# Kernel optimization log

Hardware: AMD Instinct MI355X
Metric: run time of the kernel (lower is better)

The kernel has to match this reference:

```python
import jax, jax.numpy as jnp
import numpy as np

STRIDE = 2

def setup_inputs() -> dict:
    key = jax.random.key(0)
    k1, k2 = jax.random.split(key)
    x = jax.random.normal(k1, (4, 64, 16, 16, 16), dtype=jnp.float32)
    weight = jax.random.normal(k2, (32, 64, 3, 3, 3), dtype=jnp.float32)
    return {"x": x, "weight": weight}


def reference(x, weight):
    # Faithful to ConvTranspose3dMPS.forward:
    # 1) nearest-neighbor upsample by `stride` via repeat
    # 2) per (out,in) channel pair: circular conv via FFT, summed over in
    B, C, D, H, W = x.shape
    s = STRIDE
    Co, Ci, k, _, _ = weight.shape
    Du, Hu, Wu = D * s, H * s, W * s

    # view->repeat->view == repeat each voxel s times along each spatial axis
    xu = jnp.repeat(jnp.repeat(jnp.repeat(x, s, axis=2), s, axis=3), s, axis=4)

    # FFT of upsampled input (computed once, not per channel pair)
    fx = jnp.fft.fftn(xu, axes=(2, 3, 4))  # [B, Ci, Du, Hu, Wu] complex

    # torch.fft.fftn(weight[i,j], s=x.shape[-3:]) zero-pads kernel at the end
    wpad = jnp.zeros((Co, Ci, Du, Hu, Wu), dtype=weight.dtype)
    wpad = wpad.at[:, :, :k, :k, :k].set(weight)
    fw = jnp.fft.fftn(wpad, axes=(2, 3, 4))  # [Co, Ci, Du, Hu, Wu] complex

    # sum over input channels in frequency domain, take real part of ifft
    fo = jnp.einsum('bjdhw,ijdhw->bidhw', fx, fw)
    out = jnp.fft.ifftn(fo, axes=(2, 3, 4)).real.astype(x.dtype)
    return out
```

## Files before the change

### kernel.cpp

```cpp
#include <hip/hip_runtime.h>


typedef float f32x16 __attribute__((ext_vector_type(16)));
typedef short s16x8 __attribute__((ext_vector_type(8)));

#define CI  64
#define CO  32
#define QV  4096
#define XT_ELEMS (4 * QV * CI)
#define WE_PP    (16 * 8 * 32 * 8)
#define WE_BYTES 65536
#define X_BYTES  81920
#define LDS_BYTES (WE_BYTES + X_BYTES)

__device__ __forceinline__ unsigned short f32_to_bf16_rne(float f) {
    union { float f; unsigned u; } v; v.f = f;
    unsigned u = v.u;
    unsigned r = u + 0x7FFFu + ((u >> 16) & 1u);
    return (unsigned short)(r >> 16);
}

__device__ __forceinline__ void gload_lds16(const void* g, void* l) {
    __builtin_amdgcn_global_load_lds(
        (__attribute__((address_space(1))) unsigned int*)g,
        (__attribute__((address_space(3))) unsigned int*)l, 16, 0, 0);
}

__global__ __launch_bounds__(256)
void prep_kernel(const float* __restrict__ x, const float* __restrict__ weight,
                 unsigned short* __restrict__ xT, unsigned short* __restrict__ WeG) {
    const int blk = blockIdx.x;
    {
        const int tid = blk * 256 + threadIdx.x;
        const int b  = tid >> 15;
        const int rem = tid & 32767;
        const int c  = rem >> 12;
        const int q  = rem & 4095;
        const float* xb = x + b * (CI * QV) + q;
        s16x8 pk;
        #pragma unroll
        for (int e = 0; e < 8; ++e)
            pk[e] = (short)f32_to_bf16_rne(xb[(c * 8 + e) * QV]);
        *reinterpret_cast<s16x8*>(xT + (((size_t)(b * 8 + c)) * QV + q) * 8) = pk;
    }
    if (threadIdx.x < 32) {
        const int tid = blk * 32 + threadIdx.x;
        const int p = tid >> 11, i = (tid >> 6) & 31, j = tid & 63;
        const int pd = p >> 2, ph = (p >> 1) & 1, pw = p & 1;
        const int pp = pd * 2 + ph;

        const float* wp = weight + (i * CI + j) * 27;
        float wv[27];
        #pragma unroll
        for (int k = 0; k < 27; ++k) wv[k] = wp[k];

        float t1[2][9];
        #pragma unroll
        for (int m = 0; m < 9; ++m) {
            t1[0][m] = pd ? (wv[m] + wv[9 + m]) : wv[m];
            t1[1][m] = pd ? wv[18 + m] : (wv[9 + m] + wv[18 + m]);
        }
        float t2[2][2][3];
        #pragma unroll
        for (int td = 0; td < 2; ++td)
            #pragma unroll
            for (int m = 0; m < 3; ++m) {
                t2[td][0][m] = ph ? (t1[td][m] + t1[td][3 + m]) : t1[td][m];
                t2[td][1][m] = ph ? (t1[td][6 + m]) : (t1[td][3 + m] + t1[td][6 + m]);
            }

        const int c = j >> 3, e = j & 7;
        #pragma unroll
        for (int td = 0; td < 2; ++td)
            #pragma unroll
            for (int th = 0; th < 2; ++th) {
                float a0 = pw ? (t2[td][th][0] + t2[td][th][1]) : t2[td][th][0];
                float a1 = pw ? t2[td][th][2] : (t2[td][th][1] + t2[td][th][2]);
                const int tA = td * 4 + th * 2;
                const int plane0 = pw * 8 + tA;
                WeG[(((pp * 16 + plane0) * 8 + c) * 32 + i) * 8 + e]     = f32_to_bf16_rne(a0);
                WeG[(((pp * 16 + plane0 + 1) * 8 + c) * 32 + i) * 8 + e] = f32_to_bf16_rne(a1);
            }
    }
}

__global__ __launch_bounds__(256)
void convt3d_mfma_kernel(const unsigned short* __restrict__ xT,
                         const unsigned short* __restrict__ WeG,
                         float* __restrict__ out) {
    __shared__ __align__(16) char smem[LDS_BYTES];
    unsigned short* we_lds = (unsigned short*)smem;
    char* x_lds = smem + WE_BYTES;

    const int blk = blockIdx.x;
    const int pp  = blk >> 6;
    const int T2  = blk & 63;
    const int pd = pp >> 1, ph = pp & 1;
    const int qd = T2 >> 2, qhq = T2 & 3;

    const int w    = threadIdx.x >> 6;
    const int lane = threadIdx.x & 63;

    {
        const char* src = (const char*)(WeG + pp * WE_PP);
        #pragma unroll
        for (int k = 0; k < 16; ++k) {
            const int off = (w * 16 + k) * 1024 + lane * 16;
            gload_lds16(src + off, smem + off);
        }
    }
    {
        const char* srcb = (const char*)xT;
        #pragma unroll
        for (int k = 0; k < 20; ++k) {
            const int chunk = w * 20 + k;
            const int seg   = chunk * 4 + (lane >> 4);
            const int bc    = seg / 10;
            const int dhh   = seg - bc * 10;
            const int dd_i  = (dhh >= 5) ? 1 : 0;
            const int hh_i  = dhh - dd_i * 5;
            const int dd = (qd - 1 + dd_i) & 15;
            const int hh = (qhq * 4 - 1 + hh_i) & 15;
            const long srcoff = ((long)bc * QV + (dd * 16 + hh) * 16 + (lane & 15)) * 16;
            gload_lds16(srcb + srcoff, x_lds + chunk * 1024 + lane * 16);
        }
    }
    asm volatile("s_waitcnt vmcnt(0)" ::: "memory");
    __syncthreads();

    const int b    = w;
    const int n    = lane & 31;
    const int half = lane >> 5;
    const int qw   = n & 15;
    const int hsel = n >> 4;

    f32x16 acc00 = {}, acc01 = {};
    f32x16 acc10 = {}, acc11 = {};

    #pragma unroll
    for (int t = 0; t < 8; ++t) {
        const int td = t >> 2, th = (t >> 1) & 1, tw = t & 1;
        const int dd_i = 1 - td;
        const int ww = (qw - tw) & 15;
        const int hbase = dd_i * 5 + hsel + 1 - th;
        #pragma unroll
        for (int ks = 0; ks < 4; ++ks) {
            const int c  = 2 * ks + half;
            const int bc = b * 8 + c;
            const s16x8 b0 = *reinterpret_cast<const s16x8*>(
                x_lds + (bc * 10 + hbase) * 256 + ww * 16);
            const s16x8 b1 = *reinterpret_cast<const s16x8*>(
                x_lds + (bc * 10 + hbase + 2) * 256 + ww * 16);
            const s16x8 a0 = *reinterpret_cast<const s16x8*>(
                we_lds + ((t * 8 + c) * 32 + n) * 8);
            const s16x8 a1 = *reinterpret_cast<const s16x8*>(
                we_lds + (((8 + t) * 8 + c) * 32 + n) * 8);
            acc00 = __builtin_amdgcn_mfma_f32_32x32x16_bf16(a0, b0, acc00, 0, 0, 0);
            acc01 = __builtin_amdgcn_mfma_f32_32x32x16_bf16(a1, b0, acc01, 0, 0, 0);
            acc10 = __builtin_amdgcn_mfma_f32_32x32x16_bf16(a0, b1, acc10, 0, 0, 0);
            acc11 = __builtin_amdgcn_mfma_f32_32x32x16_bf16(a1, b1, acc11, 0, 0, 0);
        }
    }

    const int d = 2 * qd + pd;
    #pragma unroll
    for (int tau = 0; tau < 2; ++tau) {
        const int h = 2 * (4 * qhq + 2 * tau + hsel) + ph;
        float* ob = out + ((size_t)b * CO) * 32768 + d * 1024 + h * 32 + 2 * qw;
        #pragma unroll
        for (int r = 0; r < 16; ++r) {
            const int m = (r & 3) + 8 * (r >> 2) + 4 * half;
            float2 v;
            if (tau == 0) { v.x = acc00[r]; v.y = acc01[r]; }
            else          { v.x = acc10[r]; v.y = acc11[r]; }
            *reinterpret_cast<float2*>(ob + (size_t)m * 32768) = v;
        }
    }
}

extern "C" void kernel_launch(void* const* d_in, const int* in_sizes, int n_in,
                              void* d_out, int out_size, void* d_ws, size_t ws_size,
                              hipStream_t stream) {
    const float* x      = (const float*)d_in[0];
    const float* weight = (const float*)d_in[1];
    float* out          = (float*)d_out;

    unsigned short* xT = (unsigned short*)d_ws;
    unsigned short* We = xT + XT_ELEMS;

    prep_kernel<<<512, 256, 0, stream>>>(x, weight, xT, We);
    convt3d_mfma_kernel<<<256, 256, 0, stream>>>(xT, We, out);
}
```

Before: 18.54 us.

## Fuse input/weight bf16 prep into the MFMA conv kernel, drop prep launch

Removes the separate prep kernel and the workspace round trip. Each block now reads fp32 weights and input directly, folds the weights into parity-phase form, converts to bf16 and writes both into LDS itself. This saves a kernel launch and the global write and read of the intermediate buffers. In exchange, each of the 256 blocks recomputes its weight fold (64 x 32 x 27 floats read per block) and does strided fp32 loads of x, which duplicates work and adds latency before the MFMA loop.

```diff
diff --git a/kernel.cpp b/kernel.cpp
--- a/kernel.cpp
+++ b/kernel.cpp
@@ -7,8 +7,6 @@
 #define CI  64
 #define CO  32
 #define QV  4096
-#define XT_ELEMS (4 * QV * CI)
-#define WE_PP    (16 * 8 * 32 * 8)
 #define WE_BYTES 65536
 #define X_BYTES  81920
 #define LDS_BYTES (WE_BYTES + X_BYTES)
@@ -20,74 +18,10 @@
     return (unsigned short)(r >> 16);
 }
 
-__device__ __forceinline__ void gload_lds16(const void* g, void* l) {
-    __builtin_amdgcn_global_load_lds(
-        (__attribute__((address_space(1))) unsigned int*)g,
-        (__attribute__((address_space(3))) unsigned int*)l, 16, 0, 0);
-}
-
 __global__ __launch_bounds__(256)
-void prep_kernel(const float* __restrict__ x, const float* __restrict__ weight,
-                 unsigned short* __restrict__ xT, unsigned short* __restrict__ WeG) {
-    const int blk = blockIdx.x;
-    {
-        const int tid = blk * 256 + threadIdx.x;
-        const int b  = tid >> 15;
-        const int rem = tid & 32767;
-        const int c  = rem >> 12;
-        const int q  = rem & 4095;
-        const float* xb = x + b * (CI * QV) + q;
-        s16x8 pk;
-        #pragma unroll
-        for (int e = 0; e < 8; ++e)
-            pk[e] = (short)f32_to_bf16_rne(xb[(c * 8 + e) * QV]);
-        *reinterpret_cast<s16x8*>(xT + (((size_t)(b * 8 + c)) * QV + q) * 8) = pk;
-    }
-    if (threadIdx.x < 32) {
-        const int tid = blk * 32 + threadIdx.x;
-        const int p = tid >> 11, i = (tid >> 6) & 31, j = tid & 63;
-        const int pd = p >> 2, ph = (p >> 1) & 1, pw = p & 1;
-        const int pp = pd * 2 + ph;
-
-        const float* wp = weight + (i * CI + j) * 27;
-        float wv[27];
-        #pragma unroll
-        for (int k = 0; k < 27; ++k) wv[k] = wp[k];
-
-        float t1[2][9];
-        #pragma unroll
-        for (int m = 0; m < 9; ++m) {
-            t1[0][m] = pd ? (wv[m] + wv[9 + m]) : wv[m];
-            t1[1][m] = pd ? wv[18 + m] : (wv[9 + m] + wv[18 + m]);
-        }
-        float t2[2][2][3];
-        #pragma unroll
-        for (int td = 0; td < 2; ++td)
-            #pragma unroll
-            for (int m = 0; m < 3; ++m) {
-                t2[td][0][m] = ph ? (t1[td][m] + t1[td][3 + m]) : t1[td][m];
-                t2[td][1][m] = ph ? (t1[td][6 + m]) : (t1[td][3 + m] + t1[td][6 + m]);
-            }
-
-        const int c = j >> 3, e = j & 7;
-        #pragma unroll
-        for (int td = 0; td < 2; ++td)
-            #pragma unroll
-            for (int th = 0; th < 2; ++th) {
-                float a0 = pw ? (t2[td][th][0] + t2[td][th][1]) : t2[td][th][0];
-                float a1 = pw ? t2[td][th][2] : (t2[td][th][1] + t2[td][th][2]);
-                const int tA = td * 4 + th * 2;
-                const int plane0 = pw * 8 + tA;
-                WeG[(((pp * 16 + plane0) * 8 + c) * 32 + i) * 8 + e]     = f32_to_bf16_rne(a0);
-                WeG[(((pp * 16 + plane0 + 1) * 8 + c) * 32 + i) * 8 + e] = f32_to_bf16_rne(a1);
-            }
-    }
-}
-
-__global__ __launch_bounds__(256)
-void convt3d_mfma_kernel(const unsigned short* __restrict__ xT,
-                         const unsigned short* __restrict__ WeG,
-                         float* __restrict__ out) {
+void convt3d_fused_kernel(const float* __restrict__ x,
+                          const float* __restrict__ weight,
+                          float* __restrict__ out) {
     __shared__ __align__(16) char smem[LDS_BYTES];
     unsigned short* we_lds = (unsigned short*)smem;
     char* x_lds = smem + WE_BYTES;
@@ -102,30 +36,69 @@
     const int lane = threadIdx.x & 63;
 
     {
-        const char* src = (const char*)(WeG + pp * WE_PP);
+        const int c = threadIdx.x & 7;
+        const int i = threadIdx.x >> 3;
+        s16x8 pk[16];
         #pragma unroll
-        for (int k = 0; k < 16; ++k) {
-            const int off = (w * 16 + k) * 1024 + lane * 16;
-            gload_lds16(src + off, smem + off);
+        for (int k = 0; k < 8; ++k) {
+            const int j = c * 8 + k;
+            const float* wp = weight + (i * CI + j) * 27;
+            float wv[27];
+            #pragma unroll
+            for (int m = 0; m < 27; ++m) wv[m] = wp[m];
+
+            float t1[2][9];
+            #pragma unroll
+            for (int m = 0; m < 9; ++m) {
+                t1[0][m] = pd ? (wv[m] + wv[9 + m]) : wv[m];
+                t1[1][m] = pd ? wv[18 + m] : (wv[9 + m] + wv[18 + m]);
+            }
+            #pragma unroll
+            for (int td = 0; td < 2; ++td)
+                #pragma unroll
+                for (int th = 0; th < 2; ++th) {
+                    float w0, w1, w2;
+                    if (th == 0) {
+                        w0 = ph ? (t1[td][0] + t1[td][3]) : t1[td][0];
+                        w1 = ph ? (t1[td][1] + t1[td][4]) : t1[td][1];
+                        w2 = ph ? (t1[td][2] + t1[td][5]) : t1[td][2];
+                    } else {
+                        w0 = ph ? t1[td][6] : (t1[td][3] + t1[td][6]);
+                        w1 = ph ? t1[td][7] : (t1[td][4] + t1[td][7]);
+                        w2 = ph ? t1[td][8] : (t1[td][5] + t1[td][8]);
+                    }
+                    const int tb = td * 4 + th * 2;
+                    pk[tb + 0][k]     = (short)f32_to_bf16_rne(w0);
+                    pk[tb + 1][k]     = (short)f32_to_bf16_rne(w1 + w2);
+                    pk[8 + tb + 0][k] = (short)f32_to_bf16_rne(w0 + w1);
+                    pk[8 + tb + 1][k] = (short)f32_to_bf16_rne(w2);
+                }
+        }
+        #pragma unroll
+        for (int plane = 0; plane < 16; ++plane)
+            *reinterpret_cast<s16x8*>(we_lds + ((plane * 8 + c) * 32 + i) * 8) = pk[plane];
+    }
+
+    {
+        #pragma unroll
+        for (int k = 0; k < 20; ++k) {
+            const int seg = (w * 20 + k) * 4 + (lane >> 4);
+            const int ww  = lane & 15;
+            const int bc  = seg / 10;
+            const int dhh = seg - bc * 10;
+            const int dd_i = (dhh >= 5) ? 1 : 0;
+            const int hh_i = dhh - dd_i * 5;
+            const int dd = (qd - 1 + dd_i) & 15;
+            const int hh = (qhq * 4 - 1 + hh_i) & 15;
+            const float* src = x + (size_t)bc * 8 * QV + dd * 256 + hh * 16 + ww;
+            s16x8 pk;
+            #pragma unroll
+            for (int e = 0; e < 8; ++e)
+                pk[e] = (short)f32_to_bf16_rne(src[e * QV]);
+            *reinterpret_cast<s16x8*>(x_lds + seg * 256 + ww * 16) = pk;
         }
     }
-    {
-        const char* srcb = (const char*)xT;
-        #pragma unroll
-        for (int k = 0; k < 20; ++k) {
-            const int chunk = w * 20 + k;
-            const int seg   = chunk * 4 + (lane >> 4);
-            const int bc    = seg / 10;
-            const int dhh   = seg - bc * 10;
-            const int dd_i  = (dhh >= 5) ? 1 : 0;
-            const int hh_i  = dhh - dd_i * 5;
-            const int dd = (qd - 1 + dd_i) & 15;
-            const int hh = (qhq * 4 - 1 + hh_i) & 15;
-            const long srcoff = ((long)bc * QV + (dd * 16 + hh) * 16 + (lane & 15)) * 16;
-            gload_lds16(srcb + srcoff, x_lds + chunk * 1024 + lane * 16);
-        }
-    }
-    asm volatile("s_waitcnt vmcnt(0)" ::: "memory");
+
     __syncthreads();
 
     const int b    = w;
@@ -185,9 +158,5 @@
     const float* weight = (const float*)d_in[1];
     float* out          = (float*)d_out;
 
-    unsigned short* xT = (unsigned short*)d_ws;
-    unsigned short* We = xT + XT_ELEMS;
-
-    prep_kernel<<<512, 256, 0, stream>>>(x, weight, xT, We);
-    convt3d_mfma_kernel<<<256, 256, 0, stream>>>(xT, We, out);
+    convt3d_fused_kernel<<<256, 256, 0, stream>>>(x, weight, out);
 }
```

Measured after the change: 21.24 us. 14.6% more time.
